# Kernel tuning notes

Measured on AMD Instinct MI355X. Metric: run time of the kernel, lower is better.

Reference implementation:

```python
import jax, jax.numpy as jnp
import numpy as np

DIM = 1024
NUM_HEADS = 16
HEAD_DIM = DIM // NUM_HEADS
SCALE = HEAD_DIM ** -0.5


def setup_inputs() -> dict:
    key = jax.random.key(0)
    ks = jax.random.split(key, 11)
    B, N, M = 8, 1024, 1024
    s = DIM ** -0.5  # init scale for weights
    return {
        "x": jax.random.normal(ks[0], (B, N, DIM), jnp.float32),
        "context": jax.random.normal(ks[1], (B, M, DIM), jnp.float32),
        "Wq": jax.random.normal(ks[2], (DIM, DIM), jnp.float32) * s,
        "bq": jax.random.normal(ks[3], (DIM,), jnp.float32) * 0.01,
        "Wk": jax.random.normal(ks[4], (DIM, DIM), jnp.float32) * s,
        "bk": jax.random.normal(ks[5], (DIM,), jnp.float32) * 0.01,
        "Wv": jax.random.normal(ks[6], (DIM, DIM), jnp.float32) * s,
        "bv": jax.random.normal(ks[7], (DIM,), jnp.float32) * 0.01,
        "Wo": jax.random.normal(ks[8], (DIM, DIM), jnp.float32) * s,
        "bo": jax.random.normal(ks[9], (DIM,), jnp.float32) * 0.01,
    }


def reference(x, context, Wq, bq, Wk, bk, Wv, bv, Wo, bo):
    B, N, _ = x.shape
    M = context.shape[1]
    # Linear projections (torch Linear: x @ W.T + b; here W stored as [in, out])
    q = x @ Wq + bq            # [B, N, DIM]
    k = context @ Wk + bk      # [B, M, DIM]
    v = context @ Wv + bv      # [B, M, DIM]
    # split heads: b n (h d) -> b h n d
    q = q.reshape(B, N, NUM_HEADS, HEAD_DIM).transpose(0, 2, 1, 3)
    k = k.reshape(B, M, NUM_HEADS, HEAD_DIM).transpose(0, 2, 1, 3)
    v = v.reshape(B, M, NUM_HEADS, HEAD_DIM).transpose(0, 2, 1, 3)
    dots = jnp.einsum('bhnd,bhmd->bhnm', q, k) * SCALE
    attn = jax.nn.softmax(dots, axis=-1)
    out = jnp.einsum('bhnm,bhmd->bhnd', attn, v)   # [B, H, N, d]
    out = out.transpose(0, 2, 1, 3).reshape(B, N, DIM)  # b h n d -> b n (h d)
    return out @ Wo + bo
```

## Files before the change

kernel.cpp:

```cpp
#include <hip/hip_runtime.h>

typedef unsigned short u16;
typedef __attribute__((ext_vector_type(8))) short bf16x8;
typedef __attribute__((ext_vector_type(4))) float f32x4;
typedef __attribute__((ext_vector_type(16))) float f32x16;
typedef __attribute__((ext_vector_type(4))) unsigned u32x4;

#define MFMA16 __builtin_amdgcn_mfma_f32_16x16x32_bf16
#define MFMA32 __builtin_amdgcn_mfma_f32_32x32x16_bf16

__device__ __forceinline__ u16 f2b(float f) {
  unsigned u = __builtin_bit_cast(unsigned, f);
  u = (u + 0x7fffu + ((u >> 16) & 1u)) >> 16;
  return (u16)u;
}

__device__ __forceinline__ void gload_lds16(const u16* g, u16* l) {
  __builtin_amdgcn_global_load_lds((const __attribute__((address_space(1))) void*)g,
                                   (__attribute__((address_space(3))) void*)l, 16, 0, 0);
}

__global__ void cvt_bf16(const float* __restrict__ a, const float* __restrict__ b,
                         u16* __restrict__ oa, u16* __restrict__ ob, int n4) {
  int i = blockIdx.x * blockDim.x + threadIdx.x;
  if (i >= n4) return;
  const float* in = blockIdx.z ? b : a;
  u16* out = blockIdx.z ? ob : oa;
  float4 v = reinterpret_cast<const float4*>(in)[i];
  ushort4 o = make_ushort4(f2b(v.x), f2b(v.y), f2b(v.z), f2b(v.w));
  reinterpret_cast<ushort4*>(out)[i] = o;
}

__global__ void wtrans(const float* __restrict__ w0, const float* __restrict__ w1,
                       const float* __restrict__ w2, const float* __restrict__ w3,
                       u16* __restrict__ o0, u16* __restrict__ o1,
                       u16* __restrict__ o2, u16* __restrict__ o3) {
  const float* src = blockIdx.z == 0 ? w0 : blockIdx.z == 1 ? w1 : blockIdx.z == 2 ? w2 : w3;
  u16* dst = blockIdx.z == 0 ? o0 : blockIdx.z == 1 ? o1 : blockIdx.z == 2 ? o2 : o3;
  __shared__ float t[64][65];
  const int tid = threadIdx.x;
  const int r0 = blockIdx.y * 64, c0 = blockIdx.x * 64;
  #pragma unroll
  for (int it = 0; it < 4; ++it) {
    int row = it * 16 + (tid >> 4);
    int col = (tid & 15) * 4;
    float4 v = *reinterpret_cast<const float4*>(&src[(size_t)(r0 + row) * 1024 + c0 + col]);
    t[row][col] = v.x; t[row][col + 1] = v.y; t[row][col + 2] = v.z; t[row][col + 3] = v.w;
  }
  __syncthreads();
  #pragma unroll
  for (int it = 0; it < 2; ++it) {
    int c = it * 32 + (tid >> 3);
    int r8 = (tid & 7) * 8;
    u16 tmp[8];
    #pragma unroll
    for (int k = 0; k < 8; ++k) tmp[k] = f2b(t[r8 + k][c]);
    uint4 pk;
    pk.x = (unsigned)tmp[0] | ((unsigned)tmp[1] << 16);
    pk.y = (unsigned)tmp[2] | ((unsigned)tmp[3] << 16);
    pk.z = (unsigned)tmp[4] | ((unsigned)tmp[5] << 16);
    pk.w = (unsigned)tmp[6] | ((unsigned)tmp[7] << 16);
    *reinterpret_cast<uint4*>(&dst[(size_t)(c0 + c) * 1024 + r0 + r8]) = pk;
  }
}

__device__ __forceinline__ void gemm_core(const u16* __restrict__ A, const u16* __restrict__ Wt,
                                          f32x4 (&acc)[4][4], int brow, int bcol) {
  __shared__ u16 As[2][128 * 32];
  __shared__ u16 Bs[2][128 * 32];
  const int tid = threadIdx.x;
  const int lane = tid & 63;
  const int w = tid >> 6;
  const int wr = w >> 1, wc = w & 1;
  const int l16 = lane & 15, g = lane >> 4;

  auto stage = [&](int buf, int kt) {
    #pragma unroll
    for (int it = 0; it < 2; ++it) {
      int chunk = it * 256 + tid;
      int row = chunk >> 2;
      int kk = (chunk & 3) * 8;
      gload_lds16(&A[(size_t)(brow + row) * 1024 + kt * 32 + kk],
                  &As[buf][(it * 256 + w * 64) * 8]);
      gload_lds16(&Wt[(size_t)(bcol + row) * 1024 + kt * 32 + kk],
                  &Bs[buf][(it * 256 + w * 64) * 8]);
    }
  };

  stage(0, 0);
  __syncthreads();
  int cur = 0;
  for (int kt = 0; kt < 32; ++kt) {
    if (kt < 31) stage(cur ^ 1, kt + 1);
    bf16x8 a[4], b[4];
    const int kb = g * 8;
    #pragma unroll
    for (int mi = 0; mi < 4; ++mi)
      a[mi] = *reinterpret_cast<const bf16x8*>(&As[cur][(wr * 64 + mi * 16 + l16) * 32 + kb]);
    #pragma unroll
    for (int ni = 0; ni < 4; ++ni)
      b[ni] = *reinterpret_cast<const bf16x8*>(&Bs[cur][(wc * 64 + ni * 16 + l16) * 32 + kb]);
    #pragma unroll
    for (int mi = 0; mi < 4; ++mi)
      #pragma unroll
      for (int ni = 0; ni < 4; ++ni)
        acc[mi][ni] = MFMA16(a[mi], b[ni], acc[mi][ni], 0, 0, 0);
    __syncthreads();
    cur ^= 1;
  }
}

__global__ __launch_bounds__(256, 2) void gemm_qkv(const u16* __restrict__ xb, const u16* __restrict__ cb,
                                                   const u16* __restrict__ Wqt, const u16* __restrict__ Wkt,
                                                   const u16* __restrict__ Wvt,
                                                   const float* __restrict__ bq, const float* __restrict__ bk,
                                                   const float* __restrict__ bv,
                                                   u16* __restrict__ Qb, u16* __restrict__ Kb,
                                                   u16* __restrict__ Vt) {
  const int z = blockIdx.z;
  const u16* A = z == 0 ? xb : cb;
  const u16* W = z == 0 ? Wqt : z == 1 ? Wkt : Wvt;
  const float* bias = z == 0 ? bq : z == 1 ? bk : bv;
  const int brow = blockIdx.x * 128, bcol = blockIdx.y * 128;
  f32x4 acc[4][4] = {};
  gemm_core(A, W, acc, brow, bcol);

  const int lane = threadIdx.x & 63;
  const int w = threadIdx.x >> 6;
  const int wr = w >> 1, wc = w & 1;
  const int l16 = lane & 15, g = lane >> 4;
  const float CS = 0.125f * 1.44269504089f;
  #pragma unroll
  for (int ni = 0; ni < 4; ++ni) {
    const int col = bcol + wc * 64 + ni * 16 + l16;
    const float bz = bias[col];
    #pragma unroll
    for (int mi = 0; mi < 4; ++mi) {
      const int r0 = brow + wr * 64 + mi * 16 + g * 4;
      f32x4 v = acc[mi][ni];
      if (z == 0) {
        u16* o = Qb;
        #pragma unroll
        for (int j = 0; j < 4; ++j) o[(size_t)(r0 + j) * 1024 + col] = f2b((v[j] + bz) * CS);
      } else if (z == 1) {
        u16* o = Kb;
        #pragma unroll
        for (int j = 0; j < 4; ++j) o[(size_t)(r0 + j) * 1024 + col] = f2b(v[j] + bz);
      } else {
        u16* o = Vt;
        const int bb = r0 >> 10, m = r0 & 1023;
        const int h = col >> 6, d = col & 63;
        ushort4 pk = make_ushort4(f2b(v[0] + bz), f2b(v[1] + bz), f2b(v[2] + bz), f2b(v[3] + bz));
        *reinterpret_cast<ushort4*>(&o[((size_t)(bb * 16 + h) * 64 + d) * 1024 + m]) = pk;
      }
    }
  }
}

__global__ __launch_bounds__(256, 2) void gemm_o(const u16* __restrict__ A, const u16* __restrict__ Wt,
                                                 const float* __restrict__ bias, float* __restrict__ outp) {
  const int brow = blockIdx.x * 128, bcol = blockIdx.y * 128;
  f32x4 acc[4][4] = {};
  gemm_core(A, Wt, acc, brow, bcol);
  const int lane = threadIdx.x & 63;
  const int w = threadIdx.x >> 6;
  const int wr = w >> 1, wc = w & 1;
  const int l16 = lane & 15, g = lane >> 4;
  #pragma unroll
  for (int ni = 0; ni < 4; ++ni) {
    const int col = bcol + wc * 64 + ni * 16 + l16;
    const float bz = bias[col];
    #pragma unroll
    for (int mi = 0; mi < 4; ++mi) {
      const int r0 = brow + wr * 64 + mi * 16 + g * 4;
      f32x4 v = acc[mi][ni];
      #pragma unroll
      for (int j = 0; j < 4; ++j) outp[(size_t)(r0 + j) * 1024 + col] = v[j] + bz;
    }
  }
}

__global__ __launch_bounds__(256, 2) void attn2(const u16* __restrict__ Q, const u16* __restrict__ K,
                                                const u16* __restrict__ Vt, u16* __restrict__ AO) {
  __shared__ u16 Ks[2][64 * 64];
  __shared__ u16 Vs[2][64 * 64];
  const int tid = threadIdx.x, lane = tid & 63, w = tid >> 6;
  const int l32 = lane & 31, u = lane >> 5;
  const int id = blockIdx.x;
  const int v = (id & 7) * 128 + (id >> 3);
  const int qt = v & 7, h = (v >> 3) & 15, b = v >> 7;
  const int q0 = qt * 128 + w * 32;
  const int sw = l32 & 7;

  bf16x8 qf[4];
  {
    const u16* qp = &Q[(size_t)(b * 1024 + q0 + l32) * 1024 + h * 64 + u * 8];
    #pragma unroll
    for (int m = 0; m < 4; ++m) qf[m] = *reinterpret_cast<const bf16x8*>(qp + m * 16);
  }

  f32x16 o0 = {}, o1 = {};
  float lr = 0.f;

  const u16* Kg = K + (size_t)(b * 1024) * 1024 + h * 64;
  const u16* Vg = Vt + (size_t)(b * 16 + h) * 64 * 1024;

  auto stage = [&](int buf, int kt) {
    #pragma unroll
    for (int i = 0; i < 2; ++i) {
      int c = w * 128 + i * 64 + lane;
      int r = c >> 3;
      int gc = ((c & 7) ^ (r & 7)) * 8;
      gload_lds16(&Kg[(size_t)(kt * 64 + r) * 1024 + gc], &Ks[buf][(w * 128 + i * 64) * 8]);
      gload_lds16(&Vg[(size_t)r * 1024 + kt * 64 + gc], &Vs[buf][(w * 128 + i * 64) * 8]);
    }
  };

  stage(0, 0);
  __syncthreads();
  int cur = 0;

  for (int kt = 0; kt < 16; ++kt) {
    if (kt < 15) stage(cur ^ 1, kt + 1);

    f32x16 s0 = {}, s1 = {};
    __builtin_amdgcn_s_setprio(1);
    #pragma unroll
    for (int m = 0; m < 4; ++m) {
      bf16x8 k0 = *reinterpret_cast<const bf16x8*>(&Ks[cur][(size_t)l32 * 64 + (((2 * m + u) ^ sw) * 8)]);
      bf16x8 k1 = *reinterpret_cast<const bf16x8*>(&Ks[cur][(size_t)(32 + l32) * 64 + (((2 * m + u) ^ sw) * 8)]);
      s0 = MFMA32(k0, qf[m], s0, 0, 0, 0);
      s1 = MFMA32(k1, qf[m], s1, 0, 0, 0);
    }
    __builtin_amdgcn_s_setprio(0);

    unsigned W0[8], W1[8];
    #pragma unroll
    for (int j = 0; j < 8; ++j) {
      const int r = 4 * (j >> 1) + 2 * (j & 1);
      float pa0 = __builtin_amdgcn_exp2f(s0[r]);
      float pb0 = __builtin_amdgcn_exp2f(s0[r + 1]);
      float pa1 = __builtin_amdgcn_exp2f(s1[r]);
      float pb1 = __builtin_amdgcn_exp2f(s1[r + 1]);
      lr += (pa0 + pb0) + (pa1 + pb1);
      asm("v_cvt_pk_bf16_f32 %0, %1, %2" : "=v"(W0[j]) : "v"(pa0), "v"(pb0));
      asm("v_cvt_pk_bf16_f32 %0, %1, %2" : "=v"(W1[j]) : "v"(pa1), "v"(pb1));
    }

    unsigned paw[4][4];
    #pragma unroll
    for (int ks = 0; ks < 4; ++ks) {
      const int ksl = ks & 1;
      #pragma unroll
      for (int p = 0; p < 2; ++p) {
        unsigned x = (ks < 2) ? W0[4 * ksl + p] : W1[4 * ksl + p];
        unsigned y = (ks < 2) ? W0[4 * ksl + 2 + p] : W1[4 * ksl + 2 + p];
        asm("v_permlane32_swap_b32 %0, %1" : "+v"(x), "+v"(y));
        paw[ks][p] = x;
        paw[ks][2 + p] = y;
      }
    }

    __builtin_amdgcn_s_setprio(1);
    #pragma unroll
    for (int ks = 0; ks < 4; ++ks) {
      bf16x8 pa = __builtin_bit_cast(bf16x8, u32x4{paw[ks][0], paw[ks][1], paw[ks][2], paw[ks][3]});
      bf16x8 v0 = *reinterpret_cast<const bf16x8*>(&Vs[cur][(size_t)l32 * 64 + (((2 * ks + u) ^ sw) * 8)]);
      bf16x8 v1 = *reinterpret_cast<const bf16x8*>(&Vs[cur][(size_t)(32 + l32) * 64 + (((2 * ks + u) ^ sw) * 8)]);
      o0 = MFMA32(pa, v0, o0, 0, 0, 0);
      o1 = MFMA32(pa, v1, o1, 0, 0, 0);
    }
    __builtin_amdgcn_s_setprio(0);

    __syncthreads();
    cur ^= 1;
  }

  float sum = lr + __shfl_xor(lr, 32);
  float rinv = 1.0f / sum;
  u16* aop = &AO[(size_t)(b * 1024 + q0) * 1024 + h * 64 + l32];
  #pragma unroll
  for (int r = 0; r < 16; ++r) {
    const int ql = (r & 3) + 8 * (r >> 2) + 4 * u;
    int ri_i = __builtin_amdgcn_ds_bpermute((ql + (u << 5)) << 2, __builtin_bit_cast(int, rinv));
    float ri = __builtin_bit_cast(float, ri_i);
    aop[(size_t)ql * 1024] = f2b(o0[r] * ri);
    aop[(size_t)ql * 1024 + 32] = f2b(o1[r] * ri);
  }
}

extern "C" void kernel_launch(void* const* d_in, const int* in_sizes, int n_in,
                              void* d_out, int out_size, void* d_ws, size_t ws_size,
                              hipStream_t stream) {
  const float* x   = (const float*)d_in[0];
  const float* ctx = (const float*)d_in[1];
  const float* Wq  = (const float*)d_in[2];
  const float* bq  = (const float*)d_in[3];
  const float* Wk  = (const float*)d_in[4];
  const float* bk  = (const float*)d_in[5];
  const float* Wv  = (const float*)d_in[6];
  const float* bv  = (const float*)d_in[7];
  const float* Wo  = (const float*)d_in[8];
  const float* bo  = (const float*)d_in[9];
  float* out = (float*)d_out;
  char* ws = (char*)d_ws;

  u16* xb  = (u16*)(ws + (size_t)0);
  u16* cb  = (u16*)(ws + ((size_t)16 << 20));
  u16* Qb  = (u16*)(ws + ((size_t)32 << 20));
  u16* Kb  = (u16*)(ws + ((size_t)48 << 20));
  u16* Vt  = (u16*)(ws + ((size_t)64 << 20));
  u16* Wqt = (u16*)(ws + ((size_t)80 << 20));
  u16* Wkt = (u16*)(ws + ((size_t)82 << 20));
  u16* Wvt = (u16*)(ws + ((size_t)84 << 20));
  u16* Wot = (u16*)(ws + ((size_t)86 << 20));

  const int n4 = (8 * 1024 * 1024) / 4;
  cvt_bf16<<<dim3(8192, 1, 2), 256, 0, stream>>>(x, ctx, xb, cb, n4);
  wtrans<<<dim3(16, 16, 4), 256, 0, stream>>>(Wq, Wk, Wv, Wo, Wqt, Wkt, Wvt, Wot);

  gemm_qkv<<<dim3(64, 8, 3), 256, 0, stream>>>(xb, cb, Wqt, Wkt, Wvt, bq, bk, bv, Qb, Kb, Vt);
  attn2<<<dim3(1024), 256, 0, stream>>>(Qb, Kb, Vt, xb );
  gemm_o<<<dim3(64, 8), 256, 0, stream>>>(xb, Wot, bo, out);
}
```

Baseline: 171.7 us.

## Double GEMM K-tile depth and stage V transpose through LDS

The shared GEMM core now loads 64-wide K tiles (two 32-wide sub-slabs) per stage, which halves the number of barrier-separated iterations and doubles the data in flight per stage. LDS is passed in as one shared buffer of 64 KB per block. The V-projection epilogue first writes its transposed tile into that LDS buffer, then emits coalesced 16-byte rows to Vt instead of scattered 8-byte stores. The larger LDS footprint may limit how many blocks fit on each CU, and the padded staging adds some LDS traffic.

```diff
diff --git a/kernel.cpp b/kernel.cpp
--- a/kernel.cpp
+++ b/kernel.cpp
@@ -65,9 +65,8 @@
 }
 
 __device__ __forceinline__ void gemm_core(const u16* __restrict__ A, const u16* __restrict__ Wt,
-                                          f32x4 (&acc)[4][4], int brow, int bcol) {
-  __shared__ u16 As[2][128 * 32];
-  __shared__ u16 Bs[2][128 * 32];
+                                          f32x4 (&acc)[4][4], int brow, int bcol,
+                                          u16* __restrict__ smem) {
   const int tid = threadIdx.x;
   const int lane = tid & 63;
   const int w = tid >> 6;
@@ -76,35 +75,42 @@
 
   auto stage = [&](int buf, int kt) {
     #pragma unroll
-    for (int it = 0; it < 2; ++it) {
-      int chunk = it * 256 + tid;
-      int row = chunk >> 2;
-      int kk = (chunk & 3) * 8;
-      gload_lds16(&A[(size_t)(brow + row) * 1024 + kt * 32 + kk],
-                  &As[buf][(it * 256 + w * 64) * 8]);
-      gload_lds16(&Wt[(size_t)(bcol + row) * 1024 + kt * 32 + kk],
-                  &Bs[buf][(it * 256 + w * 64) * 8]);
+    for (int it = 0; it < 4; ++it) {
+      int c = it * 256 + tid;
+      int row = (c >> 2) & 127;
+      int ks = c >> 9;
+      int k8 = c & 3;
+      const size_t gofs = (size_t)kt * 64 + ks * 32 + k8 * 8;
+      gload_lds16(&A[(size_t)(brow + row) * 1024 + gofs],
+                  &smem[buf * 8192 + (it * 256 + w * 64) * 8]);
+      gload_lds16(&Wt[(size_t)(bcol + row) * 1024 + gofs],
+                  &smem[16384 + buf * 8192 + (it * 256 + w * 64) * 8]);
     }
   };
 
   stage(0, 0);
   __syncthreads();
   int cur = 0;
-  for (int kt = 0; kt < 32; ++kt) {
-    if (kt < 31) stage(cur ^ 1, kt + 1);
-    bf16x8 a[4], b[4];
-    const int kb = g * 8;
-    #pragma unroll
-    for (int mi = 0; mi < 4; ++mi)
-      a[mi] = *reinterpret_cast<const bf16x8*>(&As[cur][(wr * 64 + mi * 16 + l16) * 32 + kb]);
-    #pragma unroll
-    for (int ni = 0; ni < 4; ++ni)
-      b[ni] = *reinterpret_cast<const bf16x8*>(&Bs[cur][(wc * 64 + ni * 16 + l16) * 32 + kb]);
-    #pragma unroll
-    for (int mi = 0; mi < 4; ++mi)
+  for (int kt = 0; kt < 16; ++kt) {
+    if (kt < 15) stage(cur ^ 1, kt + 1);
+    const u16* As = &smem[cur * 8192];
+    const u16* Bs = &smem[16384 + cur * 8192];
+    #pragma unroll
+    for (int ks = 0; ks < 2; ++ks) {
+      bf16x8 a[4], b[4];
+      const int kb = ks * 4096 + g * 8;
+      #pragma unroll
+      for (int mi = 0; mi < 4; ++mi)
+        a[mi] = *reinterpret_cast<const bf16x8*>(&As[kb + (wr * 64 + mi * 16 + l16) * 32]);
       #pragma unroll
       for (int ni = 0; ni < 4; ++ni)
-        acc[mi][ni] = MFMA16(a[mi], b[ni], acc[mi][ni], 0, 0, 0);
+        b[ni] = *reinterpret_cast<const bf16x8*>(&Bs[kb + (wc * 64 + ni * 16 + l16) * 32]);
+      #pragma unroll
+      for (int mi = 0; mi < 4; ++mi)
+        #pragma unroll
+        for (int ni = 0; ni < 4; ++ni)
+          acc[mi][ni] = MFMA16(a[mi], b[ni], acc[mi][ni], 0, 0, 0);
+    }
     __syncthreads();
     cur ^= 1;
   }
@@ -117,51 +123,73 @@
                                                    const float* __restrict__ bv,
                                                    u16* __restrict__ Qb, u16* __restrict__ Kb,
                                                    u16* __restrict__ Vt) {
+  __shared__ u16 smem[32768];
   const int z = blockIdx.z;
   const u16* A = z == 0 ? xb : cb;
   const u16* W = z == 0 ? Wqt : z == 1 ? Wkt : Wvt;
   const float* bias = z == 0 ? bq : z == 1 ? bk : bv;
   const int brow = blockIdx.x * 128, bcol = blockIdx.y * 128;
   f32x4 acc[4][4] = {};
-  gemm_core(A, W, acc, brow, bcol);
+  gemm_core(A, W, acc, brow, bcol, smem);
 
   const int lane = threadIdx.x & 63;
   const int w = threadIdx.x >> 6;
   const int wr = w >> 1, wc = w & 1;
   const int l16 = lane & 15, g = lane >> 4;
   const float CS = 0.125f * 1.44269504089f;
-  #pragma unroll
-  for (int ni = 0; ni < 4; ++ni) {
-    const int col = bcol + wc * 64 + ni * 16 + l16;
-    const float bz = bias[col];
-    #pragma unroll
-    for (int mi = 0; mi < 4; ++mi) {
-      const int r0 = brow + wr * 64 + mi * 16 + g * 4;
-      f32x4 v = acc[mi][ni];
-      if (z == 0) {
-        u16* o = Qb;
+
+  if (z < 2) {
+    u16* o = z == 0 ? Qb : Kb;
+    #pragma unroll
+    for (int ni = 0; ni < 4; ++ni) {
+      const int col = bcol + wc * 64 + ni * 16 + l16;
+      const float bz = bias[col];
+      #pragma unroll
+      for (int mi = 0; mi < 4; ++mi) {
+        const int r0 = brow + wr * 64 + mi * 16 + g * 4;
+        f32x4 v = acc[mi][ni];
         #pragma unroll
-        for (int j = 0; j < 4; ++j) o[(size_t)(r0 + j) * 1024 + col] = f2b((v[j] + bz) * CS);
-      } else if (z == 1) {
-        u16* o = Kb;
+        for (int j = 0; j < 4; ++j) {
+          float val = v[j] + bz;
+          if (z == 0) val *= CS;
+          o[(size_t)(r0 + j) * 1024 + col] = f2b(val);
+        }
+      }
+    }
+  } else {
+    u16* T = &smem[w * 4608];
+    #pragma unroll
+    for (int ni = 0; ni < 4; ++ni) {
+      const int col = bcol + wc * 64 + ni * 16 + l16;
+      const float bz = bias[col];
+      #pragma unroll
+      for (int mi = 0; mi < 4; ++mi) {
+        f32x4 v = acc[mi][ni];
         #pragma unroll
-        for (int j = 0; j < 4; ++j) o[(size_t)(r0 + j) * 1024 + col] = f2b(v[j] + bz);
-      } else {
-        u16* o = Vt;
-        const int bb = r0 >> 10, m = r0 & 1023;
-        const int h = col >> 6, d = col & 63;
-        ushort4 pk = make_ushort4(f2b(v[0] + bz), f2b(v[1] + bz), f2b(v[2] + bz), f2b(v[3] + bz));
-        *reinterpret_cast<ushort4*>(&o[((size_t)(bb * 16 + h) * 64 + d) * 1024 + m]) = pk;
+        for (int j = 0; j < 4; ++j)
+          T[(ni * 16 + l16) * 72 + mi * 16 + g * 4 + j] = f2b(v[j] + bz);
       }
+    }
+    const int h = (bcol + wc * 64) >> 6;
+    const int m0 = brow + wr * 64;
+    const int bb = m0 >> 10, mloc = m0 & 1023;
+    u16* vb = &Vt[((size_t)(bb * 16 + h) * 64) * 1024 + mloc];
+    #pragma unroll
+    for (int it = 0; it < 8; ++it) {
+      const int d = it * 8 + (lane >> 3);
+      const int m8 = (lane & 7) * 8;
+      bf16x8 val = *reinterpret_cast<const bf16x8*>(&T[d * 72 + m8]);
+      *reinterpret_cast<bf16x8*>(&vb[(size_t)d * 1024 + m8]) = val;
     }
   }
 }
 
 __global__ __launch_bounds__(256, 2) void gemm_o(const u16* __restrict__ A, const u16* __restrict__ Wt,
                                                  const float* __restrict__ bias, float* __restrict__ outp) {
+  __shared__ u16 smem[32768];
   const int brow = blockIdx.x * 128, bcol = blockIdx.y * 128;
   f32x4 acc[4][4] = {};
-  gemm_core(A, Wt, acc, brow, bcol);
+  gemm_core(A, Wt, acc, brow, bcol, smem);
   const int lane = threadIdx.x & 63;
   const int w = threadIdx.x >> 6;
   const int wr = w >> 1, wc = w & 1;
```

After: 152.4 us. 11.3% less time.
